# Performance work log

Hardware: AMD Instinct MI355X
Metric: run time of the kernel (lower is better)

The kernel has to match this reference:

```python
import jax, jax.numpy as jnp
import numpy as np

B, N, DIM, HID = 32, 10000, 64, 128


def _linear_params(key, fan_in, fan_out):
    kw, kb = jax.random.split(key)
    bound = 1.0 / np.sqrt(fan_in)
    w = jax.random.uniform(kw, (fan_out, fan_in), jnp.float32, -bound, bound)
    b = jax.random.uniform(kb, (fan_out,), jnp.float32, -bound, bound)
    return w, b


def setup_inputs() -> dict:
    key = jax.random.key(0)
    ks = jax.random.split(key, 7)
    x = jax.random.normal(ks[0], (B, N, DIM), jnp.float32)
    adj_col = jax.random.uniform(ks[1], (N,), jnp.float32)
    n2e_w, n2e_b = _linear_params(ks[2], 2 * DIM, HID)
    e2e_w, e2e_b = _linear_params(ks[3], HID, HID)
    e2n_w, e2n_b = _linear_params(ks[4], HID, HID)
    n2n_w, n2n_b = _linear_params(ks[5], HID, HID)
    out_w, out_b = _linear_params(ks[6], DIM + HID, DIM)
    return {
        "x": x, "adj_col": adj_col,
        "n2e_w": n2e_w, "n2e_b": n2e_b,
        "e2e_w": e2e_w, "e2e_b": e2e_b,
        "e2n_w": e2n_w, "e2n_b": e2n_b,
        "n2n_w": n2n_w, "n2n_b": n2n_b,
        "out_w": out_w, "out_b": out_b,
        "i": 5, "num": 4, "node_size": 2000,
    }


def reference(x, adj_col, n2e_w, n2e_b, e2e_w, e2e_b, e2n_w, e2n_b,
              n2n_w, n2n_b, out_w, out_b, i, num, node_size):
    # The torch loop over (num+1) chunks is an execution tiling; mathematically it
    # computes a full sum over all N nodes. We vectorize it in one pass.
    starter = x[:, i, :]                                   # [B, dim]
    ender = jnp.broadcast_to(starter[:, None, :], x.shape)  # [B, N, dim]
    c = jnp.concatenate([x, ender], axis=-1)               # [B, N, 2*dim]
    h = jax.nn.relu(jnp.einsum('bnd,hd->bnh', c, n2e_w) + n2e_b)
    h = jax.nn.relu(jnp.einsum('bnh,gh->bng', h, e2e_w) + e2e_b)
    h = h * adj_col[None, :, None]                         # adjacency mask
    s = jnp.sum(h, axis=1)                                 # [B, hid]
    y = jax.nn.relu(s @ e2n_w.T + e2n_b)
    y = jax.nn.relu(y @ n2n_w.T + n2n_b)
    out = jnp.concatenate([starter, y], axis=-1) @ out_w.T + out_b  # [B, dim]
    return out
```

## Files before the change

### kernel.cpp

```cpp
#include <hip/hip_runtime.h>
#include <hip/hip_bf16.h>

typedef float f32x4 __attribute__((ext_vector_type(4)));
typedef short bf16x8 __attribute__((ext_vector_type(8)));
typedef unsigned short u16;
typedef unsigned int u32;

#define NB 32
#define NN 10000
#define DIMX 64

__device__ __forceinline__ u32 pkbf(float a, float b) {
    __hip_bfloat162 h = __float22bfloat162_rn(make_float2(a, b));
    u32 r; __builtin_memcpy(&r, &h, 4); return r;
}

__global__ __launch_bounds__(256, 3) void k_fused(
        const float* __restrict__ x, const float* __restrict__ adj,
        const float* __restrict__ n2e_w, const float* __restrict__ n2e_b,
        const float* __restrict__ e2e_w, const float* __restrict__ e2e_b,
        const int* __restrict__ ip,
        float* __restrict__ partials) {
    __shared__ u16 sW1[8192];
    __shared__ u16 sH1[16384];
    __shared__ float sBias[256];
    __shared__ float sAdj[448];

    const int tid = threadIdx.x;
    const int lane = tid & 63, wave = tid >> 6;
    const int c = lane & 15, g = lane >> 4;
    const int bid = blockIdx.x;
    const int b = bid / 24, qb = bid - b * 24;
    const int s0 = qb ? 27 + (qb - 1) * 26 : 0;
    const int cnt = qb ? 26 : 27;
    const int i0 = ip[0];

    #pragma unroll
    for (int p = 0; p < 4; ++p) {
        int fp = p * 256 + tid;
        int f = fp >> 6, ln = fp & 63;
        int t = f >> 1, kk = f & 1;
        int row = t * 16 + (ln & 15), col = kk * 32 + (ln >> 4) * 8;
        const float* src = n2e_w + row * 128 + col;
        f32x4 lo = *(const f32x4*)src, hi = *(const f32x4*)(src + 4);
        union { bf16x8 v; u32 w[4]; } u;
        u.w[0] = pkbf(lo[0], lo[1]); u.w[1] = pkbf(lo[2], lo[3]);
        u.w[2] = pkbf(hi[0], hi[1]); u.w[3] = pkbf(hi[2], hi[3]);
        *(bf16x8*)&sW1[fp * 8] = u.v;
    }
    bf16x8 w2r[2][4];
    #pragma unroll
    for (int tt = 0; tt < 2; ++tt)
        #pragma unroll
        for (int kk2 = 0; kk2 < 4; ++kk2) {
            int row = (wave * 2 + tt) * 16 + c, col = kk2 * 32 + g * 8;
            const float* src = e2e_w + row * 128 + col;
            f32x4 lo = *(const f32x4*)src, hi = *(const f32x4*)(src + 4);
            union { bf16x8 v; u32 w[4]; } u;
            u.w[0] = pkbf(lo[0], lo[1]); u.w[1] = pkbf(lo[2], lo[3]);
            u.w[2] = pkbf(hi[0], hi[1]); u.w[3] = pkbf(hi[2], hi[3]);
            w2r[tt][kk2] = u.v;
        }
    if (tid < 128) {
        const float* xr = x + ((size_t)b * NN + i0) * DIMX;
        const float* w = n2e_w + tid * 128 + 64;
        float s = n2e_b[tid];
        #pragma unroll 16
        for (int d = 0; d < 64; ++d) s += xr[d] * w[d];
        sBias[tid] = s;
    } else {
        sBias[tid] = e2e_b[tid - 128];
    }
    for (int idx = tid; idx < 448; idx += 256)
        sAdj[idx] = (idx < cnt * 16) ? adj[s0 * 16 + idx] : 0.f;

    float sAcc[2] = {0.f, 0.f};
    __syncthreads();

    const size_t xbatch = (size_t)b * NN;
    const int swzW = 16 * (c & 3);
    const int rdOff = (c * 64 + 16 * (g ^ (c & 3))) >> 1;

    f32x4 xl[4];
    {
        int idx = wave;
        int stl = idx < cnt ? idx : cnt - 1;
        const float* xr = x + (xbatch + (s0 + stl) * 16 + c) * 64 + g * 8;
        xl[0] = *(const f32x4*)(xr);
        xl[1] = *(const f32x4*)(xr + 4);
        xl[2] = *(const f32x4*)(xr + 32);
        xl[3] = *(const f32x4*)(xr + 36);
    }

    int par = 0;
    #pragma unroll 1
    for (int it = 0; it < 7; ++it) {
        bf16x8 A1[2];
        #pragma unroll
        for (int kk = 0; kk < 2; ++kk) {
            f32x4 lo = xl[kk * 2], hi = xl[kk * 2 + 1];
            union { bf16x8 v; u32 w[4]; } u;
            u.w[0] = pkbf(lo[0], lo[1]); u.w[1] = pkbf(lo[2], lo[3]);
            u.w[2] = pkbf(hi[0], hi[1]); u.w[3] = pkbf(hi[2], hi[3]);
            A1[kk] = u.v;
        }
        if (it < 6) {
            int idx = (it + 1) * 4 + wave;
            int stl = idx < cnt ? idx : cnt - 1;
            const float* xr = x + (xbatch + (s0 + stl) * 16 + c) * 64 + g * 8;
            xl[0] = *(const f32x4*)(xr);
            xl[1] = *(const f32x4*)(xr + 4);
            xl[2] = *(const f32x4*)(xr + 32);
            xl[3] = *(const f32x4*)(xr + 36);
        }

        u16* const bufW = &sH1[par * 8192 + wave * 512];
        #pragma unroll
        for (int kk2 = 0; kk2 < 4; ++kk2) {
            const int t0 = kk2 * 2, t1 = kk2 * 2 + 1;
            bf16x8 w1a0 = *(const bf16x8*)&sW1[(t0 * 2 + 0) * 512 + lane * 8];
            bf16x8 w1b0 = *(const bf16x8*)&sW1[(t0 * 2 + 1) * 512 + lane * 8];
            bf16x8 w1a1 = *(const bf16x8*)&sW1[(t1 * 2 + 0) * 512 + lane * 8];
            bf16x8 w1b1 = *(const bf16x8*)&sW1[(t1 * 2 + 1) * 512 + lane * 8];
            f32x4 cb0 = *(const f32x4*)&sBias[t0 * 16 + 4 * g];
            f32x4 cb1 = *(const f32x4*)&sBias[t1 * 16 + 4 * g];
            f32x4 d0 = __builtin_amdgcn_mfma_f32_16x16x32_bf16(w1a0, A1[0], cb0, 0, 0, 0);
            d0 = __builtin_amdgcn_mfma_f32_16x16x32_bf16(w1b0, A1[1], d0, 0, 0, 0);
            f32x4 d1 = __builtin_amdgcn_mfma_f32_16x16x32_bf16(w1a1, A1[0], cb1, 0, 0, 0);
            d1 = __builtin_amdgcn_mfma_f32_16x16x32_bf16(w1b1, A1[1], d1, 0, 0, 0);
            u32 p00 = pkbf(fmaxf(d0[0], 0.f), fmaxf(d0[1], 0.f));
            u32 p01 = pkbf(fmaxf(d0[2], 0.f), fmaxf(d0[3], 0.f));
            u32 p10 = pkbf(fmaxf(d1[0], 0.f), fmaxf(d1[1], 0.f));
            u32 p11 = pkbf(fmaxf(d1[2], 0.f), fmaxf(d1[3], 0.f));
            int base = c * 64;
            *(uint2*)&bufW[kk2 * 2048 + ((base + ((8 * g) ^ swzW)) >> 1)]      = make_uint2(p00, p01);
            *(uint2*)&bufW[kk2 * 2048 + ((base + ((32 + 8 * g) ^ swzW)) >> 1)] = make_uint2(p10, p11);
        }
        __syncthreads();

        f32x4 acc[4][2];
        #pragma unroll
        for (int sub = 0; sub < 4; ++sub)
            #pragma unroll
            for (int tt = 0; tt < 2; ++tt) acc[sub][tt] = (f32x4){0.f,0.f,0.f,0.f};
        const u16* const bufR = &sH1[par * 8192];
        #pragma unroll
        for (int kk2 = 0; kk2 < 4; ++kk2) {
            bf16x8 A2[4];
            #pragma unroll
            for (int sub = 0; sub < 4; ++sub)
                A2[sub] = *(const bf16x8*)&bufR[kk2 * 2048 + sub * 512 + rdOff];
            #pragma unroll
            for (int tt = 0; tt < 2; ++tt)
                #pragma unroll
                for (int sub = 0; sub < 4; ++sub)
                    acc[sub][tt] = __builtin_amdgcn_mfma_f32_16x16x32_bf16(A2[sub], w2r[tt][kk2], acc[sub][tt], 0, 0, 0);
        }

        #pragma unroll
        for (int tt = 0; tt < 2; ++tt) {
            float bb = sBias[128 + (wave * 2 + tt) * 16 + c];
            #pragma unroll
            for (int sub = 0; sub < 4; ++sub) {
                f32x4 av = *(const f32x4*)&sAdj[(it * 4 + sub) * 16 + 4 * g];
                #pragma unroll
                for (int r = 0; r < 4; ++r)
                    sAcc[tt] = fmaf(av[r], fmaxf(acc[sub][tt][r] + bb, 0.f), sAcc[tt]);
            }
        }
        par ^= 1;
    }

    float red[2];
    #pragma unroll
    for (int tt = 0; tt < 2; ++tt) {
        float v = sAcc[tt];
        v += __shfl_xor(v, 16, 64);
        v += __shfl_xor(v, 32, 64);
        red[tt] = v;
    }
    if (lane < 16) {
        #pragma unroll
        for (int tt = 0; tt < 2; ++tt)
            partials[bid * 128 + (wave * 2 + tt) * 16 + lane] = red[tt];
    }
}

__global__ void k_final(const float* __restrict__ partials, const float* __restrict__ x,
                        const int* __restrict__ ip,
                        const float* __restrict__ e2n_w, const float* __restrict__ e2n_b,
                        const float* __restrict__ n2n_w, const float* __restrict__ n2n_b,
                        const float* __restrict__ out_w, const float* __restrict__ out_b,
                        float* __restrict__ out) {
    int b = blockIdx.x, j = threadIdx.x;
    __shared__ float s0[128], s1[128], s2[128];
    float acc = 0.f;
    #pragma unroll
    for (int qq = 0; qq < 24; ++qq) acc += partials[(b * 24 + qq) * 128 + j];
    s0[j] = acc;
    __syncthreads();
    {
        float a1 = e2n_b[j];
        const float* w = e2n_w + j * 128;
        #pragma unroll 8
        for (int k = 0; k < 128; ++k) a1 += w[k] * s0[k];
        s1[j] = fmaxf(a1, 0.f);
    }
    __syncthreads();
    {
        float a2 = n2n_b[j];
        const float* w = n2n_w + j * 128;
        #pragma unroll 8
        for (int k = 0; k < 128; ++k) a2 += w[k] * s1[k];
        s2[j] = fmaxf(a2, 0.f);
    }
    __syncthreads();
    if (j < 64) {
        int i = ip[0];
        const float* xr = x + ((size_t)b * NN + i) * DIMX;
        const float* ow = out_w + j * 192;
        float o = out_b[j];
        #pragma unroll 8
        for (int m = 0; m < 64; ++m) o += ow[m] * xr[m];
        #pragma unroll 8
        for (int m = 0; m < 128; ++m) o += ow[64 + m] * s2[m];
        out[b * 64 + j] = o;
    }
}

extern "C" void kernel_launch(void* const* d_in, const int* in_sizes, int n_in,
                              void* d_out, int out_size, void* d_ws, size_t ws_size,
                              hipStream_t stream) {
    const float* x      = (const float*)d_in[0];
    const float* adj    = (const float*)d_in[1];
    const float* n2e_w  = (const float*)d_in[2];
    const float* n2e_b  = (const float*)d_in[3];
    const float* e2e_w  = (const float*)d_in[4];
    const float* e2e_b  = (const float*)d_in[5];
    const float* e2n_w  = (const float*)d_in[6];
    const float* e2n_b  = (const float*)d_in[7];
    const float* n2n_w  = (const float*)d_in[8];
    const float* n2n_b  = (const float*)d_in[9];
    const float* out_w  = (const float*)d_in[10];
    const float* out_b  = (const float*)d_in[11];
    const int*   ip     = (const int*)d_in[12];
    float* out = (float*)d_out;

    float* partials = (float*)d_ws;

    k_fused<<<768, 256, 0, stream>>>(x, adj, n2e_w, n2e_b, e2e_w, e2e_b,
                                     ip, partials);
    k_final<<<32, 128, 0, stream>>>(partials, x, ip, e2n_w, e2n_b, n2n_w, n2n_b,
                                    out_w, out_b, out);
}
```

Measured before the change: 50.15 us.

## Split each batch over 32 blocks and single-buffer the hidden tile

Grid grows from 768 to 1024 blocks (32 per batch, 19-20 sixteen-node tiles each, 5 iterations instead of 7), giving finer work splitting across CUs. The double-buffered sH1 becomes a single buffer with an extra barrier after the second GEMM reads, halving that LDS use to help occupancy. The starter bias dot product is now split across all 256 threads with a shuffle reduction instead of 128 threads doing 64-length loops. The cost is a second __syncthreads per iteration and more partials for the final kernel to sum.

```diff
diff --git a/kernel.cpp b/kernel.cpp
--- a/kernel.cpp
+++ b/kernel.cpp
@@ -15,24 +15,24 @@
     u32 r; __builtin_memcpy(&r, &h, 4); return r;
 }
 
-__global__ __launch_bounds__(256, 3) void k_fused(
+__global__ __launch_bounds__(256, 3) void k_main(
         const float* __restrict__ x, const float* __restrict__ adj,
         const float* __restrict__ n2e_w, const float* __restrict__ n2e_b,
         const float* __restrict__ e2e_w, const float* __restrict__ e2e_b,
         const int* __restrict__ ip,
         float* __restrict__ partials) {
     __shared__ u16 sW1[8192];
-    __shared__ u16 sH1[16384];
+    __shared__ u16 sH1[8192];
     __shared__ float sBias[256];
-    __shared__ float sAdj[448];
+    __shared__ float sAdj[320];
 
     const int tid = threadIdx.x;
     const int lane = tid & 63, wave = tid >> 6;
     const int c = lane & 15, g = lane >> 4;
     const int bid = blockIdx.x;
-    const int b = bid / 24, qb = bid - b * 24;
-    const int s0 = qb ? 27 + (qb - 1) * 26 : 0;
-    const int cnt = qb ? 26 : 27;
+    const int b = bid >> 5, qb = bid & 31;
+    const int s0 = qb < 17 ? qb * 20 : 340 + (qb - 17) * 19;
+    const int cnt = qb < 17 ? 20 : 19;
     const int i0 = ip[0];
 
     #pragma unroll
@@ -61,17 +61,18 @@
             u.w[2] = pkbf(hi[0], hi[1]); u.w[3] = pkbf(hi[2], hi[3]);
             w2r[tt][kk2] = u.v;
         }
-    if (tid < 128) {
-        const float* xr = x + ((size_t)b * NN + i0) * DIMX;
-        const float* w = n2e_w + tid * 128 + 64;
-        float s = n2e_b[tid];
-        #pragma unroll 16
-        for (int d = 0; d < 64; ++d) s += xr[d] * w[d];
-        sBias[tid] = s;
-    } else {
-        sBias[tid] = e2e_b[tid - 128];
-    }
-    for (int idx = tid; idx < 448; idx += 256)
+    {
+        int j = tid >> 1, half = tid & 1;
+        const float* xr = x + ((size_t)b * NN + i0) * DIMX + half * 32;
+        const float* w = n2e_w + j * 128 + 64 + half * 32;
+        float s = 0.f;
+        #pragma unroll 8
+        for (int d = 0; d < 32; ++d) s += xr[d] * w[d];
+        s += __shfl_xor(s, 1, 64);
+        if (!half) sBias[j] = s + n2e_b[j];
+    }
+    if (tid < 128) sBias[128 + tid] = e2e_b[tid];
+    for (int idx = tid; idx < 320; idx += 256)
         sAdj[idx] = (idx < cnt * 16) ? adj[s0 * 16 + idx] : 0.f;
 
     float sAcc[2] = {0.f, 0.f};
@@ -92,9 +93,8 @@
         xl[3] = *(const f32x4*)(xr + 36);
     }
 
-    int par = 0;
     #pragma unroll 1
-    for (int it = 0; it < 7; ++it) {
+    for (int it = 0; it < 5; ++it) {
         bf16x8 A1[2];
         #pragma unroll
         for (int kk = 0; kk < 2; ++kk) {
@@ -104,7 +104,7 @@
             u.w[2] = pkbf(hi[0], hi[1]); u.w[3] = pkbf(hi[2], hi[3]);
             A1[kk] = u.v;
         }
-        if (it < 6) {
+        if (it < 4) {
             int idx = (it + 1) * 4 + wave;
             int stl = idx < cnt ? idx : cnt - 1;
             const float* xr = x + (xbatch + (s0 + stl) * 16 + c) * 64 + g * 8;
@@ -114,7 +114,7 @@
             xl[3] = *(const f32x4*)(xr + 36);
         }
 
-        u16* const bufW = &sH1[par * 8192 + wave * 512];
+        u16* const bufW = &sH1[wave * 512];
         #pragma unroll
         for (int kk2 = 0; kk2 < 4; ++kk2) {
             const int t0 = kk2 * 2, t1 = kk2 * 2 + 1;
@@ -143,19 +143,19 @@
         for (int sub = 0; sub < 4; ++sub)
             #pragma unroll
             for (int tt = 0; tt < 2; ++tt) acc[sub][tt] = (f32x4){0.f,0.f,0.f,0.f};
-        const u16* const bufR = &sH1[par * 8192];
         #pragma unroll
         for (int kk2 = 0; kk2 < 4; ++kk2) {
             bf16x8 A2[4];
             #pragma unroll
             for (int sub = 0; sub < 4; ++sub)
-                A2[sub] = *(const bf16x8*)&bufR[kk2 * 2048 + sub * 512 + rdOff];
+                A2[sub] = *(const bf16x8*)&sH1[kk2 * 2048 + sub * 512 + rdOff];
             #pragma unroll
             for (int tt = 0; tt < 2; ++tt)
                 #pragma unroll
                 for (int sub = 0; sub < 4; ++sub)
                     acc[sub][tt] = __builtin_amdgcn_mfma_f32_16x16x32_bf16(A2[sub], w2r[tt][kk2], acc[sub][tt], 0, 0, 0);
         }
+        __syncthreads();
 
         #pragma unroll
         for (int tt = 0; tt < 2; ++tt) {
@@ -168,7 +168,6 @@
                     sAcc[tt] = fmaf(av[r], fmaxf(acc[sub][tt][r] + bb, 0.f), sAcc[tt]);
             }
         }
-        par ^= 1;
     }
 
     float red[2];
@@ -196,7 +195,7 @@
     __shared__ float s0[128], s1[128], s2[128];
     float acc = 0.f;
     #pragma unroll
-    for (int qq = 0; qq < 24; ++qq) acc += partials[(b * 24 + qq) * 128 + j];
+    for (int qq = 0; qq < 32; ++qq) acc += partials[(b * 32 + qq) * 128 + j];
     s0[j] = acc;
     __syncthreads();
     {
@@ -248,7 +247,7 @@
 
     float* partials = (float*)d_ws;
 
-    k_fused<<<768, 256, 0, stream>>>(x, adj, n2e_w, n2e_b, e2e_w, e2e_b,
+    k_main<<<1024, 256, 0, stream>>>(x, adj, n2e_w, n2e_b, e2e_w, e2e_b,
                                      ip, partials);
     k_final<<<32, 128, 0, stream>>>(partials, x, ip, e2n_w, e2n_b, n2n_w, n2n_b,
                                     out_w, out_b, out);
```

New measurement: 52.34 us. 1.04x slower.
